# Performance work log

Hardware: AMD Instinct MI355X
Metric: run time of the kernel (lower is better)

The kernel has to match this reference:

```python
import jax, jax.numpy as jnp
import numpy as np
import math


def _local_band_mask(L):
    # window_size = ceil(1.2 * log2(L) / 2); True where attention is DISALLOWED
    w = math.ceil(1.2 * np.log2(L) / 2)
    i = jnp.arange(L)[:, None]
    j = jnp.arange(L)[None, :]
    return jnp.abs(i - j) > w  # [L, L] bool, True outside the band


def setup_inputs() -> dict:
    key = jax.random.key(0)
    kq, kk, kv = jax.random.split(key, 3)
    B, L, H, E = 2, 2048, 8, 64
    return {
        "queries": jax.random.normal(kq, (B, L, H, E), dtype=jnp.float32),
        "keys": jax.random.normal(kk, (B, L, H, E), dtype=jnp.float32),
        "values": jax.random.normal(kv, (B, L, H, E), dtype=jnp.float32),
    }


def reference(queries, keys, values):
    # queries/keys: [B, L, H, E], values: [B, L, H, D]
    B, L, H, E = queries.shape
    scale = 1.0 / math.sqrt(E)
    # scores: [B, H, L, L]
    scores = jnp.einsum("bqhe,bkhe->bhqk", queries, keys) * scale
    mask = _local_band_mask(L)  # [L, L]
    scores = jnp.where(mask[None, None, :, :], -jnp.inf, scores)
    attn = jax.nn.softmax(scores, axis=-1)  # dropout is identity in eval
    # output: [B, L, H, D]
    out = jnp.einsum("bhqk,bkhd->bqhd", attn, values)
    return out
```

## Files before the change

kernel.cpp:

```cpp
#include <hip/hip_runtime.h>
#include <math.h>


constexpr int L_DIM = 2048;
constexpr int H_DIM = 8;
constexpr int E_DIM = 64;
constexpr int W = 7;
constexpr int NK = 2 * W + 1;
constexpr int TQ = 64;
constexpr int HALO = 8;
constexpr int ROWS = TQ + 2 * HALO;

template <int CTRL>
__device__ __forceinline__ float dpp_add(float s) {
  int t = __builtin_amdgcn_mov_dpp(__builtin_bit_cast(int, s), CTRL, 0xF, 0xF, true);
  return s + __builtin_bit_cast(float, t);
}

__global__ __launch_bounds__(512, 4) void local_attn_kernel(
    const float* __restrict__ q,
    const float* __restrict__ k,
    const float* __restrict__ v,
    float* __restrict__ out) {
  __shared__ float ks[ROWS * E_DIM];
  __shared__ float vs[ROWS * E_DIM];

  const int cpx = gridDim.x >> 3;
  const int bid = (blockIdx.x & 7) * cpx + (blockIdx.x >> 3);

  const int tile = bid & (L_DIM / TQ - 1);
  const int bh = bid >> 5;
  const int h = bh & (H_DIM - 1);
  const int b = bh >> 3;
  const int l0 = tile * TQ;

  const int tid = threadIdx.x;
  const int wv = tid >> 6;
  const int lane = tid & 63;
  const int qsub = lane >> 3;
  const int c = lane & 7;

  const size_t bhb = (size_t)b * L_DIM * H_DIM + h;

  const int rsub = lane >> 4;
  const int c4 = lane & 15;
  float4 stg[5];
  int stg_slot[5];
#pragma unroll
  for (int t = 0; t < 5; ++t) {
    const int ch = wv + t * 8;
    const int m = (ch >= 20) ? 1 : 0;
    const int cc = ch - m * 20;
    const int rl = cc * 4 + rsub;
    int rg = l0 - HALO + rl;
    rg = rg < 0 ? 0 : (rg > L_DIM - 1 ? L_DIM - 1 : rg);
    const float* src =
        (m ? v : k) + ((bhb + (size_t)rg * H_DIM) << 6) + c4 * 4;
    stg[t] = *(const float4*)src;
    stg_slot[t] = rl * 16 + (c4 ^ (rl & 7));
  }

  const int l0w = l0 + wv * 8;
  const int l = l0w + qsub;
  const float* qp = q + ((bhb + (size_t)l * H_DIM) << 6) + c * 8;
  float4 q0 = *(const float4*)qp;
  float4 q1 = *(const float4*)(qp + 4);
  const float scale = 0.125f;
  q0.x *= scale; q0.y *= scale; q0.z *= scale; q0.w *= scale;
  q1.x *= scale; q1.y *= scale; q1.z *= scale; q1.w *= scale;

#pragma unroll
  for (int t = 0; t < 5; ++t) {
    const int ch = wv + t * 8;
    float* dst = ((ch >= 20) ? vs : ks) + stg_slot[t] * 4;
    *(float4*)dst = stg[t];
  }
  __syncthreads();

  const int base_rl = wv * 8 + 1 + qsub;
  float sc[NK];
#pragma unroll
  for (int j = 0; j < NK; ++j) {
    const int rl = base_rl + j;
    const int s8 = rl & 7;
    const float4 k0 = *(const float4*)&ks[(rl * 16 + ((2 * c) ^ s8)) * 4];
    const float4 k1 = *(const float4*)&ks[(rl * 16 + ((2 * c + 1) ^ s8)) * 4];
    float s = q0.x * k0.x + q0.y * k0.y + q0.z * k0.z + q0.w * k0.w +
              q1.x * k1.x + q1.y * k1.y + q1.z * k1.z + q1.w * k1.w;
    s = dpp_add<0xB1>(s);
    s = dpp_add<0x4E>(s);
    s = dpp_add<0x141>(s);
    const int kk = l0w + qsub - W + j;
    sc[j] = ((unsigned)kk < (unsigned)L_DIM) ? s : -INFINITY;
  }

  float mx = sc[0];
#pragma unroll
  for (int j = 1; j < NK; ++j) mx = fmaxf(mx, sc[j]);
  float den = 0.0f;
#pragma unroll
  for (int j = 0; j < NK; ++j) {
    sc[j] = __expf(sc[j] - mx);
    den += sc[j];
  }
  const float inv = __builtin_amdgcn_rcpf(den);

  float4 a0 = {0.f, 0.f, 0.f, 0.f};
  float4 a1 = {0.f, 0.f, 0.f, 0.f};
#pragma unroll
  for (int j = 0; j < NK; ++j) {
    const int rl = base_rl + j;
    const int s8 = rl & 7;
    const float4 v0 = *(const float4*)&vs[(rl * 16 + ((2 * c) ^ s8)) * 4];
    const float4 v1 = *(const float4*)&vs[(rl * 16 + ((2 * c + 1) ^ s8)) * 4];
    const float p = sc[j];
    a0.x += p * v0.x; a0.y += p * v0.y; a0.z += p * v0.z; a0.w += p * v0.w;
    a1.x += p * v1.x; a1.y += p * v1.y; a1.z += p * v1.z; a1.w += p * v1.w;
  }

  float* op = out + ((bhb + (size_t)l * H_DIM) << 6) + c * 8;
  a0.x *= inv; a0.y *= inv; a0.z *= inv; a0.w *= inv;
  a1.x *= inv; a1.y *= inv; a1.z *= inv; a1.w *= inv;
  *(float4*)op = a0;
  *(float4*)(op + 4) = a1;
}

extern "C" void kernel_launch(void* const* d_in, const int* in_sizes, int n_in,
                              void* d_out, int out_size, void* d_ws, size_t ws_size,
                              hipStream_t stream) {
  const float* q = (const float*)d_in[0];
  const float* k = (const float*)d_in[1];
  const float* v = (const float*)d_in[2];
  float* out = (float*)d_out;

  const int B = in_sizes[0] / (L_DIM * H_DIM * E_DIM);
  const int blocks = B * H_DIM * (L_DIM / TQ);

  local_attn_kernel<<<blocks, 512, 0, stream>>>(q, k, v, out);
}
```

Baseline: 12.27 us.

## Halve query tile and split K/V staging to overlap V store with scores

Query tile shrinks from 64 to 32 rows with 256-thread blocks, which doubles the block count and raises the halo re-read fraction. K and V loads are both issued up front, but only K goes to shared memory before the first barrier. V is written to shared memory after the softmax, behind a second barrier, so its latency can overlap the score computation. The cost is an extra barrier and more halo traffic.

```diff
diff --git a/kernel.cpp b/kernel.cpp
--- a/kernel.cpp
+++ b/kernel.cpp
@@ -7,9 +7,10 @@
 constexpr int E_DIM = 64;
 constexpr int W = 7;
 constexpr int NK = 2 * W + 1;
-constexpr int TQ = 64;
+constexpr int TQ = 32;
 constexpr int HALO = 8;
 constexpr int ROWS = TQ + 2 * HALO;
+constexpr int NCH = ROWS / 4;
 
 template <int CTRL>
 __device__ __forceinline__ float dpp_add(float s) {
@@ -17,7 +18,7 @@
   return s + __builtin_bit_cast(float, t);
 }
 
-__global__ __launch_bounds__(512, 4) void local_attn_kernel(
+__global__ __launch_bounds__(256, 4) void local_attn_kernel(
     const float* __restrict__ q,
     const float* __restrict__ k,
     const float* __restrict__ v,
@@ -29,7 +30,7 @@
   const int bid = (blockIdx.x & 7) * cpx + (blockIdx.x >> 3);
 
   const int tile = bid & (L_DIM / TQ - 1);
-  const int bh = bid >> 5;
+  const int bh = bid >> 6;
   const int h = bh & (H_DIM - 1);
   const int b = bh >> 3;
   const int l0 = tile * TQ;
@@ -44,38 +45,39 @@
 
   const int rsub = lane >> 4;
   const int c4 = lane & 15;
-  float4 stg[5];
-  int stg_slot[5];
+
+  int rl_s[3], slot_s[3];
+  const float* ksrc[3];
 #pragma unroll
-  for (int t = 0; t < 5; ++t) {
-    const int ch = wv + t * 8;
-    const int m = (ch >= 20) ? 1 : 0;
-    const int cc = ch - m * 20;
+  for (int t = 0; t < 3; ++t) {
+    const int cc = wv + t * 4;
     const int rl = cc * 4 + rsub;
     int rg = l0 - HALO + rl;
     rg = rg < 0 ? 0 : (rg > L_DIM - 1 ? L_DIM - 1 : rg);
-    const float* src =
-        (m ? v : k) + ((bhb + (size_t)rg * H_DIM) << 6) + c4 * 4;
-    stg[t] = *(const float4*)src;
-    stg_slot[t] = rl * 16 + (c4 ^ (rl & 7));
+    rl_s[t] = rl;
+    slot_s[t] = rl * 16 + (c4 ^ (rl & 7));
+    ksrc[t] = k + ((bhb + (size_t)rg * H_DIM) << 6) + c4 * 4;
   }
 
+  float4 stgK[3], stgV[3];
+#pragma unroll
+  for (int t = 0; t < 3; ++t) stgK[t] = *(const float4*)ksrc[t];
+#pragma unroll
+  for (int t = 0; t < 3; ++t)
+    stgV[t] = *(const float4*)(v + (ksrc[t] - k));
   const int l0w = l0 + wv * 8;
   const int l = l0w + qsub;
   const float* qp = q + ((bhb + (size_t)l * H_DIM) << 6) + c * 8;
   float4 q0 = *(const float4*)qp;
   float4 q1 = *(const float4*)(qp + 4);
+
+#pragma unroll
+  for (int t = 0; t < 3; ++t) *(float4*)&ks[slot_s[t] * 4] = stgK[t];
+  __syncthreads();
+
   const float scale = 0.125f;
   q0.x *= scale; q0.y *= scale; q0.z *= scale; q0.w *= scale;
   q1.x *= scale; q1.y *= scale; q1.z *= scale; q1.w *= scale;
-
-#pragma unroll
-  for (int t = 0; t < 5; ++t) {
-    const int ch = wv + t * 8;
-    float* dst = ((ch >= 20) ? vs : ks) + stg_slot[t] * 4;
-    *(float4*)dst = stg[t];
-  }
-  __syncthreads();
 
   const int base_rl = wv * 8 + 1 + qsub;
   float sc[NK];
@@ -104,6 +106,10 @@
     den += sc[j];
   }
   const float inv = __builtin_amdgcn_rcpf(den);
+
+#pragma unroll
+  for (int t = 0; t < 3; ++t) *(float4*)&vs[slot_s[t] * 4] = stgV[t];
+  __syncthreads();
 
   float4 a0 = {0.f, 0.f, 0.f, 0.f};
   float4 a1 = {0.f, 0.f, 0.f, 0.f};
@@ -136,5 +142,5 @@
   const int B = in_sizes[0] / (L_DIM * H_DIM * E_DIM);
   const int blocks = B * H_DIM * (L_DIM / TQ);
 
-  local_attn_kernel<<<blocks, 512, 0, stream>>>(q, k, v, out);
+  local_attn_kernel<<<blocks, 256, 0, stream>>>(q, k, v, out);
 }
```

Result: slower. 15.02 us (+22.4%).

## Split K/V staging across waves and defer V shared-memory stores past softmax

Applied to the files above, without the earlier changes.

Waves 0-3 now load K rows and waves 4-7 load V rows, instead of each wave loading an interleaved mix. K is written to LDS before a first barrier, and V is written only after the scores and softmax, behind a second barrier, so the V global loads can finish while QK and softmax run. Launch bounds drop to 2 blocks per CU, which gives more registers for holding the staged V data, but it adds a barrier and may lower occupancy.

```diff
diff --git a/kernel.cpp b/kernel.cpp
--- a/kernel.cpp
+++ b/kernel.cpp
@@ -17,7 +17,7 @@
   return s + __builtin_bit_cast(float, t);
 }
 
-__global__ __launch_bounds__(512, 4) void local_attn_kernel(
+__global__ __launch_bounds__(512, 2) void local_attn_kernel(
     const float* __restrict__ q,
     const float* __restrict__ k,
     const float* __restrict__ v,
@@ -44,20 +44,19 @@
 
   const int rsub = lane >> 4;
   const int c4 = lane & 15;
+  const bool isK = (wv < 4);
+  const int cbase = (isK ? wv : (wv - 4)) * 5;
+  const float* mat = isK ? k : v;
+
   float4 stg[5];
-  int stg_slot[5];
+  int slot_s[5];
 #pragma unroll
   for (int t = 0; t < 5; ++t) {
-    const int ch = wv + t * 8;
-    const int m = (ch >= 20) ? 1 : 0;
-    const int cc = ch - m * 20;
-    const int rl = cc * 4 + rsub;
+    const int rl = (cbase + t) * 4 + rsub;
     int rg = l0 - HALO + rl;
     rg = rg < 0 ? 0 : (rg > L_DIM - 1 ? L_DIM - 1 : rg);
-    const float* src =
-        (m ? v : k) + ((bhb + (size_t)rg * H_DIM) << 6) + c4 * 4;
-    stg[t] = *(const float4*)src;
-    stg_slot[t] = rl * 16 + (c4 ^ (rl & 7));
+    slot_s[t] = rl * 16 + (c4 ^ (rl & 7));
+    stg[t] = *(const float4*)(mat + ((bhb + (size_t)rg * H_DIM) << 6) + c4 * 4);
   }
 
   const int l0w = l0 + wv * 8;
@@ -65,17 +64,18 @@
   const float* qp = q + ((bhb + (size_t)l * H_DIM) << 6) + c * 8;
   float4 q0 = *(const float4*)qp;
   float4 q1 = *(const float4*)(qp + 4);
+
+  if (isK) {
+#pragma unroll
+    for (int t = 0; t < 5; ++t) *(float4*)&ks[slot_s[t] * 4] = stg[t];
+  }
+  asm volatile("s_waitcnt lgkmcnt(0)" ::: "memory");
+  __builtin_amdgcn_s_barrier();
+  __builtin_amdgcn_sched_barrier(0);
+
   const float scale = 0.125f;
   q0.x *= scale; q0.y *= scale; q0.z *= scale; q0.w *= scale;
   q1.x *= scale; q1.y *= scale; q1.z *= scale; q1.w *= scale;
-
-#pragma unroll
-  for (int t = 0; t < 5; ++t) {
-    const int ch = wv + t * 8;
-    float* dst = ((ch >= 20) ? vs : ks) + stg_slot[t] * 4;
-    *(float4*)dst = stg[t];
-  }
-  __syncthreads();
 
   const int base_rl = wv * 8 + 1 + qsub;
   float sc[NK];
@@ -104,6 +104,15 @@
     den += sc[j];
   }
   const float inv = __builtin_amdgcn_rcpf(den);
+
+  __builtin_amdgcn_sched_barrier(0);
+  if (!isK) {
+#pragma unroll
+    for (int t = 0; t < 5; ++t) *(float4*)&vs[slot_s[t] * 4] = stg[t];
+  }
+  asm volatile("s_waitcnt lgkmcnt(0)" ::: "memory");
+  __builtin_amdgcn_s_barrier();
+  __builtin_amdgcn_sched_barrier(0);
 
   float4 a0 = {0.f, 0.f, 0.f, 0.f};
   float4 a1 = {0.f, 0.f, 0.f, 0.f};
```

Result: slower. 17.70 us (+44.3%).
